# Kernel tuning notes

Measured on AMD Instinct MI355X. Metric: run time of the kernel, lower is better.

The kernel has to match this reference:

```python
import jax, jax.numpy as jnp
import numpy as np

N = 100000
E = 3200000
IN_DIM = 256
OUT_DIM = 256
BN_EPS = 1e-5


def setup_inputs() -> dict:
    key = jax.random.key(0)
    k1, k2, k3, k4, k5 = jax.random.split(key, 5)
    x = jax.random.normal(k1, (N, IN_DIM), dtype=jnp.float32)
    edge_rows = jax.random.randint(k2, (E,), 0, N, dtype=jnp.int32)
    edge_cols = jax.random.randint(k3, (E,), 0, N, dtype=jnp.int32)
    edge_vals = jax.random.uniform(k4, (E,), dtype=jnp.float32)
    # xavier_uniform-like init for weight
    limit = float(np.sqrt(6.0 / (IN_DIM + OUT_DIM)))
    weight = jax.random.uniform(k5, (IN_DIM, OUT_DIM), minval=-limit, maxval=limit, dtype=jnp.float32)
    gamma = jnp.ones((OUT_DIM,), dtype=jnp.float32)
    beta = jnp.zeros((OUT_DIM,), dtype=jnp.float32)
    return {"x": x, "edge_rows": edge_rows, "edge_cols": edge_cols,
            "edge_vals": edge_vals, "weight": weight, "gamma": gamma, "beta": beta}


def reference(x, edge_rows, edge_cols, edge_vals, weight, gamma, beta):
    # dense projection: [N, in] @ [in, out] -> [N, out]
    z = jnp.matmul(x, weight)
    # sparse adjacency matmul (spmm): gather source rows, scale, scatter-add to dest
    msgs = edge_vals[:, None] * z[edge_cols]          # [E, out]
    agg = jax.ops.segment_sum(msgs, edge_rows, num_segments=N)  # [N, out]
    # BatchNorm1d (training mode: batch stats, biased variance) + ReLU
    mean = jnp.mean(agg, axis=0)
    var = jnp.mean(jnp.square(agg - mean), axis=0)
    norm = (agg - mean) * jax.lax.rsqrt(var + BN_EPS) * gamma + beta
    return jax.nn.relu(norm)
```

## Files before the change

### kernel.cpp

```cpp
#include <hip/hip_runtime.h>
#include <hip/hip_bf16.h>

#define N_NODES 100000
#define N_EDGES 3200000
#define DIM 256
#define BN_EPS 1e-5f
#define BROWS 256
#define NBUCK ((N_NODES + BROWS - 1) / BROWS)
#define BIN_BLOCKS 512
#define EPB (N_EDGES / BIN_BLOCKS)
#define RPW 4
#define NPART 64

typedef __attribute__((ext_vector_type(8))) short short8v;
typedef __attribute__((ext_vector_type(4))) float f32x4;

__device__ __forceinline__ float b2f(unsigned short h) {
    return __uint_as_float(((unsigned int)h) << 16);
}
__device__ __forceinline__ unsigned short f2b(float f) {
    unsigned int u = __float_as_uint(f);
    unsigned int rounded = u + 0x7FFF + ((u >> 16) & 1);
    return (unsigned short)(rounded >> 16);
}

__global__ __launch_bounds__(256) void wfrag_kernel(const float* __restrict__ W,
                                                    unsigned short* __restrict__ wfrag) {
    const int t = blockIdx.x * 256 + threadIdx.x;
    const int e = t & 7;
    const int l = (t >> 3) & 63;
    const int frag = t >> 9;
    const int nt = frag >> 3;
    const int ks = frag & 7;
    const int k = ks * 32 + ((l >> 4) << 3) + e;
    const int c = nt * 16 + (l & 15);
    wfrag[t] = f2b(W[k * DIM + c]);
}

__global__ __launch_bounds__(256) void gemm_mfma_kernel(const float* __restrict__ x,
                                                        const unsigned short* __restrict__ wfrag,
                                                        unsigned short* __restrict__ zb) {
    const int wid = (blockIdx.x * blockDim.x + threadIdx.x) >> 6;
    const int lane = threadIdx.x & 63;
    if (wid >= N_NODES / 16) return;
    const int m0 = wid * 16;

    const int arow = m0 + (lane & 15);
    const int kb = (lane >> 4) << 3;
    const float* xrow = x + (size_t)arow * DIM + kb;
    short8v af[8];
    #pragma unroll
    for (int ks = 0; ks < 8; ++ks) {
        const float4 a0 = *(const float4*)(xrow + ks * 32);
        const float4 a1 = *(const float4*)(xrow + ks * 32 + 4);
        short8v f;
        f[0] = (short)f2b(a0.x); f[1] = (short)f2b(a0.y);
        f[2] = (short)f2b(a0.z); f[3] = (short)f2b(a0.w);
        f[4] = (short)f2b(a1.x); f[5] = (short)f2b(a1.y);
        f[6] = (short)f2b(a1.z); f[7] = (short)f2b(a1.w);
        af[ks] = f;
    }

    const int drow0 = m0 + ((lane >> 4) << 2);
    const int dcol = lane & 15;
    for (int nt = 0; nt < 16; ++nt) {
        f32x4 acc = {0.f, 0.f, 0.f, 0.f};
        const unsigned short* wp = wfrag + ((size_t)(nt * 8) * 64 + lane) * 8;
        #pragma unroll
        for (int ks = 0; ks < 8; ++ks) {
            const short8v bf = *(const short8v*)(wp + (size_t)ks * 64 * 8);
            acc = __builtin_amdgcn_mfma_f32_16x16x32_bf16(af[ks], bf, acc, 0, 0, 0);
        }
        unsigned short* zp = zb + (size_t)drow0 * DIM + nt * 16 + dcol;
        zp[0]       = f2b(acc[0]);
        zp[DIM]     = f2b(acc[1]);
        zp[2 * DIM] = f2b(acc[2]);
        zp[3 * DIM] = f2b(acc[3]);
    }
}

__global__ __launch_bounds__(256) void coarse_hist_kernel(const int* __restrict__ rows,
                                                          int* __restrict__ coarse) {
    __shared__ int h[NBUCK];
    const int t = threadIdx.x;
    for (int i = t; i < NBUCK; i += 256) h[i] = 0;
    __syncthreads();
    const int stride = gridDim.x * 256;
    for (int e = blockIdx.x * 256 + t; e < N_EDGES; e += stride)
        atomicAdd(&h[rows[e] >> 8], 1);
    __syncthreads();
    for (int i = t; i < NBUCK; i += 256)
        if (h[i]) atomicAdd(&coarse[i], h[i]);
}

__global__ __launch_bounds__(512) void scan_coarse_kernel(const int* __restrict__ coarse,
                                                          int* __restrict__ coarseBase,
                                                          int* __restrict__ gCursor,
                                                          int* __restrict__ row_ptr) {
    __shared__ int s[512];
    const int t = threadIdx.x;
    const int v = (t < NBUCK) ? coarse[t] : 0;
    s[t] = v;
    __syncthreads();
    for (int off = 1; off < 512; off <<= 1) {
        int x = (t >= off) ? s[t - off] : 0;
        __syncthreads();
        s[t] += x;
        __syncthreads();
    }
    if (t < NBUCK) {
        coarseBase[t] = s[t] - v;
        gCursor[t] = s[t] - v;
    }
    if (t == 0) row_ptr[N_NODES] = N_EDGES;
}

__global__ __launch_bounds__(256) void bin_kernel(const int* __restrict__ rows,
                                                  const int* __restrict__ cols,
                                                  const float* __restrict__ vals,
                                                  int* gCursor,
                                                  int2* __restrict__ gBinned) {
    __shared__ int h[NBUCK];
    __shared__ int base[NBUCK];
    __shared__ int cur[NBUCK];
    const int t = threadIdx.x;
    const int e0 = blockIdx.x * EPB;
    for (int i = t; i < NBUCK; i += 256) h[i] = 0;
    __syncthreads();
    for (int e = e0 + t; e < e0 + EPB; e += 256)
        atomicAdd(&h[rows[e] >> 8], 1);
    __syncthreads();
    for (int b = t; b < NBUCK; b += 256) {
        cur[b] = 0;
        if (h[b]) base[b] = atomicAdd(&gCursor[b], h[b]);
    }
    __syncthreads();
    for (int e = e0 + t; e < e0 + EPB; e += 256) {
        const int r = rows[e];
        const int b = r >> 8;
        const int rk = atomicAdd(&cur[b], 1);
        int2 p;
        p.x = ((r & 255) << 17) | cols[e];
        p.y = __float_as_int(vals[e]);
        gBinned[base[b] + rk] = p;
    }
}

__global__ __launch_bounds__(256) void fine_sort_kernel(const int* __restrict__ coarse,
                                                        const int* __restrict__ coarseBase,
                                                        const int2* __restrict__ gBinned,
                                                        int* __restrict__ row_ptr,
                                                        int2* __restrict__ finalE) {
    __shared__ int h[BROWS];
    __shared__ int s[BROWS];
    __shared__ int cur[BROWS];
    const int t = threadIdx.x;
    const int b = blockIdx.x;
    const int base0 = coarseBase[b];
    const int cnt = coarse[b];
    h[t] = 0;
    __syncthreads();
    for (int e = base0 + t; e < base0 + cnt; e += 256)
        atomicAdd(&h[gBinned[e].x >> 17], 1);
    __syncthreads();
    s[t] = h[t];
    __syncthreads();
    for (int off = 1; off < BROWS; off <<= 1) {
        int x = (t >= off) ? s[t - off] : 0;
        __syncthreads();
        s[t] += x;
        __syncthreads();
    }
    const int excl = s[t] - h[t];
    const int grow = b * BROWS + t;
    if (grow < N_NODES) row_ptr[grow] = base0 + excl;
    cur[t] = excl;
    __syncthreads();
    for (int e = base0 + t; e < base0 + cnt; e += 256) {
        const int2 p = gBinned[e];
        const int rl = p.x >> 17;
        const int rk = atomicAdd(&cur[rl], 1);
        int2 q;
        q.x = p.x & 0x1FFFF;
        q.y = p.y;
        finalE[base0 + rk] = q;
    }
}

__global__ __launch_bounds__(256) void spmm_csr_kernel(const int* __restrict__ row_ptr,
                                                       const int2* __restrict__ pairs,
                                                       const unsigned short* __restrict__ zb,
                                                       float* __restrict__ out,
                                                       float* __restrict__ partials) {
    __shared__ float sdata[2 * DIM];
    const int t = threadIdx.x;
    sdata[t] = 0.f;
    sdata[t + 256] = 0.f;
    __syncthreads();

    const int wave = (blockIdx.x * 256 + t) >> 6;
    const int lane = t & 63;
    const int row0 = wave * RPW;

    float4 s  = make_float4(0.f, 0.f, 0.f, 0.f);
    float4 sq = make_float4(0.f, 0.f, 0.f, 0.f);

    for (int row = row0; row < row0 + RPW; ++row) {
        const int start = __builtin_amdgcn_readfirstlane(row_ptr[row]);
        const int end   = __builtin_amdgcn_readfirstlane(row_ptr[row + 1]);
        float4 acc = make_float4(0.f, 0.f, 0.f, 0.f);
        int2 pA[8], pB[8];
        ushort4 mA[8], mB[8];

#define LOADX(P, M, EB) do { \
    _Pragma("unroll") for (int j = 0; j < 8; ++j) P[j] = pairs[(EB) + j]; \
    _Pragma("unroll") for (int j = 0; j < 8; ++j) \
        M[j] = ((const ushort4*)(zb + (size_t)P[j].x * DIM))[lane]; \
  } while (0)
#define FMAX(P, M) do { \
    _Pragma("unroll") for (int j = 0; j < 8; ++j) { \
        const float v = __int_as_float(P[j].y); \
        acc.x += v * b2f(M[j].x); \
        acc.y += v * b2f(M[j].y); \
        acc.z += v * b2f(M[j].z); \
        acc.w += v * b2f(M[j].w); \
    } \
  } while (0)

        const int nb = (end - start) >> 3;
        int e = start;
        if (nb) {
            LOADX(pA, mA, e); e += 8;
            int b = 1;
            for (; b + 1 < nb; b += 2) {
                LOADX(pB, mB, e); e += 8;
                FMAX(pA, mA);
                LOADX(pA, mA, e); e += 8;
                FMAX(pB, mB);
            }
            if (b < nb) {
                LOADX(pB, mB, e); e += 8;
                FMAX(pA, mA);
                FMAX(pB, mB);
            } else {
                FMAX(pA, mA);
            }
        }
        const int rem = end - e;
        if (rem) {
            #pragma unroll
            for (int j = 0; j < 8; ++j) if (j < rem) pA[j] = pairs[e + j];
            #pragma unroll
            for (int j = 0; j < 8; ++j) if (j < rem)
                mA[j] = ((const ushort4*)(zb + (size_t)pA[j].x * DIM))[lane];
            #pragma unroll
            for (int j = 0; j < 8; ++j) if (j < rem) {
                const float v = __int_as_float(pA[j].y);
                acc.x += v * b2f(mA[j].x);
                acc.y += v * b2f(mA[j].y);
                acc.z += v * b2f(mA[j].z);
                acc.w += v * b2f(mA[j].w);
            }
        }
#undef LOADX
#undef FMAX

        f32x4 st = {acc.x, acc.y, acc.z, acc.w};
        __builtin_nontemporal_store(st, (f32x4*)(out + (size_t)row * DIM) + lane);

        s.x += acc.x; s.y += acc.y; s.z += acc.z; s.w += acc.w;
        sq.x += acc.x * acc.x; sq.y += acc.y * acc.y;
        sq.z += acc.z * acc.z; sq.w += acc.w * acc.w;
    }

    const int c0 = lane * 4;
    atomicAdd(&sdata[c0 + 0], s.x);
    atomicAdd(&sdata[c0 + 1], s.y);
    atomicAdd(&sdata[c0 + 2], s.z);
    atomicAdd(&sdata[c0 + 3], s.w);
    atomicAdd(&sdata[256 + c0 + 0], sq.x);
    atomicAdd(&sdata[256 + c0 + 1], sq.y);
    atomicAdd(&sdata[256 + c0 + 2], sq.z);
    atomicAdd(&sdata[256 + c0 + 3], sq.w);
    __syncthreads();

    float* pb = partials + (size_t)(blockIdx.x & (NPART - 1)) * (2 * DIM);
    atomicAdd(&pb[t], sdata[t]);
    atomicAdd(&pb[t + 256], sdata[t + 256]);
}

__global__ __launch_bounds__(256) void finalize_kernel(const float* __restrict__ partials,
                                                       const float* __restrict__ gamma,
                                                       const float* __restrict__ beta,
                                                       float* __restrict__ sb) {
    const int c = threadIdx.x;
    float s = 0.f, ssq = 0.f;
    for (int b = 0; b < NPART; ++b) {
        s   += partials[b * (2 * DIM) + c];
        ssq += partials[b * (2 * DIM) + 256 + c];
    }
    const float inv_n = 1.0f / (float)N_NODES;
    const float mean = s * inv_n;
    float var = ssq * inv_n - mean * mean;
    const float rstd = rsqrtf(var + BN_EPS);
    const float scale = rstd * gamma[c];
    sb[c] = scale;
    sb[DIM + c] = beta[c] - mean * scale;
}

#define NORM_BLOCKS 2048
__global__ __launch_bounds__(256) void norm_kernel(float* __restrict__ out,
                                                   const float* __restrict__ sb) {
    const int c0 = (threadIdx.x & 63) * 4;
    const float s0 = sb[c0 + 0], s1 = sb[c0 + 1], s2 = sb[c0 + 2], s3 = sb[c0 + 3];
    const float b0 = sb[DIM + c0 + 0], b1 = sb[DIM + c0 + 1];
    const float b2 = sb[DIM + c0 + 2], b3 = sb[DIM + c0 + 3];
    const int nvec = N_NODES * (DIM / 4);
    for (int idx = blockIdx.x * 256 + threadIdx.x; idx < nvec; idx += NORM_BLOCKS * 256) {
        float4 a = ((float4*)out)[idx];
        float4 o;
        o.x = fmaxf(fmaf(a.x, s0, b0), 0.f);
        o.y = fmaxf(fmaf(a.y, s1, b1), 0.f);
        o.z = fmaxf(fmaf(a.z, s2, b2), 0.f);
        o.w = fmaxf(fmaf(a.w, s3, b3), 0.f);
        ((float4*)out)[idx] = o;
    }
}

extern "C" void kernel_launch(void* const* d_in, const int* in_sizes, int n_in,
                              void* d_out, int out_size, void* d_ws, size_t ws_size,
                              hipStream_t stream) {
    const float* x         = (const float*)d_in[0];
    const int*   edge_rows = (const int*)d_in[1];
    const int*   edge_cols = (const int*)d_in[2];
    const float* edge_vals = (const float*)d_in[3];
    const float* weight    = (const float*)d_in[4];
    const float* gamma     = (const float*)d_in[5];
    const float* beta      = (const float*)d_in[6];
    float* out = (float*)d_out;

    unsigned short* zb    = (unsigned short*)d_ws;
    unsigned short* wfrag = zb + (size_t)N_NODES * DIM;
    int2*  gBinned  = (int2*)(wfrag + DIM * DIM);
    int2*  finalE   = gBinned + N_EDGES;
    int*   row_ptr  = (int*)(finalE + N_EDGES);
    int*   coarse   = row_ptr + N_NODES + 1;
    float* partials = (float*)(coarse + 392);
    float* sb       = partials + NPART * 2 * DIM;
    int*   coarseBase = (int*)(sb + 2 * DIM);
    int*   gCursor  = coarseBase + 392;

    hipMemsetAsync(coarse, 0, (392 + NPART * 2 * DIM) * sizeof(int), stream);

    wfrag_kernel<<<DIM * DIM / 256, 256, 0, stream>>>(weight, wfrag);
    gemm_mfma_kernel<<<(N_NODES / 16 + 3) / 4, 256, 0, stream>>>(x, wfrag, zb);

    coarse_hist_kernel<<<BIN_BLOCKS, 256, 0, stream>>>(edge_rows, coarse);
    scan_coarse_kernel<<<1, 512, 0, stream>>>(coarse, coarseBase, gCursor, row_ptr);
    bin_kernel<<<BIN_BLOCKS, 256, 0, stream>>>(edge_rows, edge_cols, edge_vals, gCursor, gBinned);
    fine_sort_kernel<<<NBUCK, 256, 0, stream>>>(coarse, coarseBase, gBinned, row_ptr, finalE);

    spmm_csr_kernel<<<N_NODES / (RPW * 4), 256, 0, stream>>>(row_ptr, finalE, zb, out, partials);

    finalize_kernel<<<1, 256, 0, stream>>>(partials, gamma, beta, sb);
    norm_kernel<<<NORM_BLOCKS, 256, 0, stream>>>(out, sb);
}
```

Baseline: 485.0 us.

## Split SpMM into two column-half passes to shrink gather working set

The CSR SpMM now runs as two launches, each handling 128 of the 256 output columns. Every lane gathers a ushort2 instead of a ushort4. The gathered slice of the bf16 feature table per pass is half as large, which is meant to improve L2/MALL hit rates on the random row gathers. In exchange the edge list and row pointers are read twice, there is an extra launch, and each gather moves fewer bytes, so per-edge overhead goes up.

```diff
diff --git a/kernel.cpp b/kernel.cpp
--- a/kernel.cpp
+++ b/kernel.cpp
@@ -14,6 +14,7 @@
 
 typedef __attribute__((ext_vector_type(8))) short short8v;
 typedef __attribute__((ext_vector_type(4))) float f32x4;
+typedef __attribute__((ext_vector_type(2))) float f32x2;
 
 __device__ __forceinline__ float b2f(unsigned short h) {
     return __uint_as_float(((unsigned int)h) << 16);
@@ -191,7 +192,8 @@
                                                        const int2* __restrict__ pairs,
                                                        const unsigned short* __restrict__ zb,
                                                        float* __restrict__ out,
-                                                       float* __restrict__ partials) {
+                                                       float* __restrict__ partials,
+                                                       const int hh) {
     __shared__ float sdata[2 * DIM];
     const int t = threadIdx.x;
     sdata[t] = 0.f;
@@ -201,29 +203,28 @@
     const int wave = (blockIdx.x * 256 + t) >> 6;
     const int lane = t & 63;
     const int row0 = wave * RPW;
-
-    float4 s  = make_float4(0.f, 0.f, 0.f, 0.f);
-    float4 sq = make_float4(0.f, 0.f, 0.f, 0.f);
+    const int cb = hh << 7;
+
+    f32x2 s  = {0.f, 0.f};
+    f32x2 sq = {0.f, 0.f};
 
     for (int row = row0; row < row0 + RPW; ++row) {
         const int start = __builtin_amdgcn_readfirstlane(row_ptr[row]);
         const int end   = __builtin_amdgcn_readfirstlane(row_ptr[row + 1]);
-        float4 acc = make_float4(0.f, 0.f, 0.f, 0.f);
+        f32x2 acc = {0.f, 0.f};
         int2 pA[8], pB[8];
-        ushort4 mA[8], mB[8];
+        ushort2 mA[8], mB[8];
 
 #define LOADX(P, M, EB) do { \
     _Pragma("unroll") for (int j = 0; j < 8; ++j) P[j] = pairs[(EB) + j]; \
     _Pragma("unroll") for (int j = 0; j < 8; ++j) \
-        M[j] = ((const ushort4*)(zb + (size_t)P[j].x * DIM))[lane]; \
+        M[j] = ((const ushort2*)(zb + (size_t)P[j].x * DIM + cb))[lane]; \
   } while (0)
 #define FMAX(P, M) do { \
     _Pragma("unroll") for (int j = 0; j < 8; ++j) { \
         const float v = __int_as_float(P[j].y); \
         acc.x += v * b2f(M[j].x); \
         acc.y += v * b2f(M[j].y); \
-        acc.z += v * b2f(M[j].z); \
-        acc.w += v * b2f(M[j].w); \
     } \
   } while (0)
 
@@ -252,41 +253,37 @@
             for (int j = 0; j < 8; ++j) if (j < rem) pA[j] = pairs[e + j];
             #pragma unroll
             for (int j = 0; j < 8; ++j) if (j < rem)
-                mA[j] = ((const ushort4*)(zb + (size_t)pA[j].x * DIM))[lane];
+                mA[j] = ((const ushort2*)(zb + (size_t)pA[j].x * DIM + cb))[lane];
             #pragma unroll
             for (int j = 0; j < 8; ++j) if (j < rem) {
                 const float v = __int_as_float(pA[j].y);
                 acc.x += v * b2f(mA[j].x);
                 acc.y += v * b2f(mA[j].y);
-                acc.z += v * b2f(mA[j].z);
-                acc.w += v * b2f(mA[j].w);
             }
         }
 #undef LOADX
 #undef FMAX
 
-        f32x4 st = {acc.x, acc.y, acc.z, acc.w};
-        __builtin_nontemporal_store(st, (f32x4*)(out + (size_t)row * DIM) + lane);
-
-        s.x += acc.x; s.y += acc.y; s.z += acc.z; s.w += acc.w;
+        __builtin_nontemporal_store(acc, (f32x2*)(out + (size_t)row * DIM + cb) + lane);
+
+        s.x += acc.x; s.y += acc.y;
         sq.x += acc.x * acc.x; sq.y += acc.y * acc.y;
-        sq.z += acc.z * acc.z; sq.w += acc.w * acc.w;
-    }
-
-    const int c0 = lane * 4;
+    }
+
+    const int c0 = cb + lane * 2;
     atomicAdd(&sdata[c0 + 0], s.x);
     atomicAdd(&sdata[c0 + 1], s.y);
-    atomicAdd(&sdata[c0 + 2], s.z);
-    atomicAdd(&sdata[c0 + 3], s.w);
     atomicAdd(&sdata[256 + c0 + 0], sq.x);
     atomicAdd(&sdata[256 + c0 + 1], sq.y);
-    atomicAdd(&sdata[256 + c0 + 2], sq.z);
-    atomicAdd(&sdata[256 + c0 + 3], sq.w);
     __syncthreads();
 
     float* pb = partials + (size_t)(blockIdx.x & (NPART - 1)) * (2 * DIM);
-    atomicAdd(&pb[t], sdata[t]);
-    atomicAdd(&pb[t + 256], sdata[t + 256]);
+    if (t < 128) {
+        atomicAdd(&pb[cb + t], sdata[cb + t]);
+    } else if (t < 256) {
+        const int i = 256 + cb + (t - 128);
+        atomicAdd(&pb[i], sdata[i]);
+    }
 }
 
 __global__ __launch_bounds__(256) void finalize_kernel(const float* __restrict__ partials,
@@ -360,7 +357,8 @@
     bin_kernel<<<BIN_BLOCKS, 256, 0, stream>>>(edge_rows, edge_cols, edge_vals, gCursor, gBinned);
     fine_sort_kernel<<<NBUCK, 256, 0, stream>>>(coarse, coarseBase, gBinned, row_ptr, finalE);
 
-    spmm_csr_kernel<<<N_NODES / (RPW * 4), 256, 0, stream>>>(row_ptr, finalE, zb, out, partials);
+    spmm_csr_kernel<<<N_NODES / (RPW * 4), 256, 0, stream>>>(row_ptr, finalE, zb, out, partials, 0);
+    spmm_csr_kernel<<<N_NODES / (RPW * 4), 256, 0, stream>>>(row_ptr, finalE, zb, out, partials, 1);
 
     finalize_kernel<<<1, 256, 0, stream>>>(partials, gamma, beta, sb);
     norm_kernel<<<NORM_BLOCKS, 256, 0, stream>>>(out, sb);
```

Result: slower. 504.4 us (+4.0%).

## Replace histogram+scan with fixed-capacity bucket slots and per-row end pointers

Applied to the files above, without the earlier changes.

Removes the coarse histogram pass and the single-block scan kernel. The bin kernel now writes each bucket of 256 rows into a fixed slot of CAP entries, using an atomic per-bucket counter as the cursor. The fine sort emits separate row_ptr and row_end arrays, and the SpMM reads its row end from row_end. The binned scratch reuses the zb workspace region, so binning runs before the GEMM. This saves one full read of edge_rows and two launches, but silently overflows if any bucket gets more than CAP edges, which could happen with skewed degree distributions.

```diff
diff --git a/kernel.cpp b/kernel.cpp
--- a/kernel.cpp
+++ b/kernel.cpp
@@ -11,6 +11,7 @@
 #define EPB (N_EDGES / BIN_BLOCKS)
 #define RPW 4
 #define NPART 64
+#define CAP 10240
 
 typedef __attribute__((ext_vector_type(8))) short short8v;
 typedef __attribute__((ext_vector_type(4))) float f32x4;
@@ -79,46 +80,10 @@
     }
 }
 
-__global__ __launch_bounds__(256) void coarse_hist_kernel(const int* __restrict__ rows,
-                                                          int* __restrict__ coarse) {
-    __shared__ int h[NBUCK];
-    const int t = threadIdx.x;
-    for (int i = t; i < NBUCK; i += 256) h[i] = 0;
-    __syncthreads();
-    const int stride = gridDim.x * 256;
-    for (int e = blockIdx.x * 256 + t; e < N_EDGES; e += stride)
-        atomicAdd(&h[rows[e] >> 8], 1);
-    __syncthreads();
-    for (int i = t; i < NBUCK; i += 256)
-        if (h[i]) atomicAdd(&coarse[i], h[i]);
-}
-
-__global__ __launch_bounds__(512) void scan_coarse_kernel(const int* __restrict__ coarse,
-                                                          int* __restrict__ coarseBase,
-                                                          int* __restrict__ gCursor,
-                                                          int* __restrict__ row_ptr) {
-    __shared__ int s[512];
-    const int t = threadIdx.x;
-    const int v = (t < NBUCK) ? coarse[t] : 0;
-    s[t] = v;
-    __syncthreads();
-    for (int off = 1; off < 512; off <<= 1) {
-        int x = (t >= off) ? s[t - off] : 0;
-        __syncthreads();
-        s[t] += x;
-        __syncthreads();
-    }
-    if (t < NBUCK) {
-        coarseBase[t] = s[t] - v;
-        gCursor[t] = s[t] - v;
-    }
-    if (t == 0) row_ptr[N_NODES] = N_EDGES;
-}
-
 __global__ __launch_bounds__(256) void bin_kernel(const int* __restrict__ rows,
                                                   const int* __restrict__ cols,
                                                   const float* __restrict__ vals,
-                                                  int* gCursor,
+                                                  int* bucketCnt,
                                                   int2* __restrict__ gBinned) {
     __shared__ int h[NBUCK];
     __shared__ int base[NBUCK];
@@ -132,7 +97,7 @@
     __syncthreads();
     for (int b = t; b < NBUCK; b += 256) {
         cur[b] = 0;
-        if (h[b]) base[b] = atomicAdd(&gCursor[b], h[b]);
+        if (h[b]) base[b] = atomicAdd(&bucketCnt[b], h[b]);
     }
     __syncthreads();
     for (int e = e0 + t; e < e0 + EPB; e += 256) {
@@ -142,22 +107,22 @@
         int2 p;
         p.x = ((r & 255) << 17) | cols[e];
         p.y = __float_as_int(vals[e]);
-        gBinned[base[b] + rk] = p;
-    }
-}
-
-__global__ __launch_bounds__(256) void fine_sort_kernel(const int* __restrict__ coarse,
-                                                        const int* __restrict__ coarseBase,
+        gBinned[(size_t)b * CAP + base[b] + rk] = p;
+    }
+}
+
+__global__ __launch_bounds__(256) void fine_sort_kernel(const int* __restrict__ bucketCnt,
                                                         const int2* __restrict__ gBinned,
                                                         int* __restrict__ row_ptr,
+                                                        int* __restrict__ row_end,
                                                         int2* __restrict__ finalE) {
     __shared__ int h[BROWS];
     __shared__ int s[BROWS];
     __shared__ int cur[BROWS];
     const int t = threadIdx.x;
     const int b = blockIdx.x;
-    const int base0 = coarseBase[b];
-    const int cnt = coarse[b];
+    const int base0 = b * CAP;
+    const int cnt = bucketCnt[b];
     h[t] = 0;
     __syncthreads();
     for (int e = base0 + t; e < base0 + cnt; e += 256)
@@ -173,7 +138,10 @@
     }
     const int excl = s[t] - h[t];
     const int grow = b * BROWS + t;
-    if (grow < N_NODES) row_ptr[grow] = base0 + excl;
+    if (grow < N_NODES) {
+        row_ptr[grow] = base0 + excl;
+        row_end[grow] = base0 + s[t];
+    }
     cur[t] = excl;
     __syncthreads();
     for (int e = base0 + t; e < base0 + cnt; e += 256) {
@@ -188,6 +156,7 @@
 }
 
 __global__ __launch_bounds__(256) void spmm_csr_kernel(const int* __restrict__ row_ptr,
+                                                       const int* __restrict__ row_end,
                                                        const int2* __restrict__ pairs,
                                                        const unsigned short* __restrict__ zb,
                                                        float* __restrict__ out,
@@ -207,7 +176,7 @@
 
     for (int row = row0; row < row0 + RPW; ++row) {
         const int start = __builtin_amdgcn_readfirstlane(row_ptr[row]);
-        const int end   = __builtin_amdgcn_readfirstlane(row_ptr[row + 1]);
+        const int end   = __builtin_amdgcn_readfirstlane(row_end[row]);
         float4 acc = make_float4(0.f, 0.f, 0.f, 0.f);
         int2 pA[8], pB[8];
         ushort4 mA[8], mB[8];
@@ -340,27 +309,24 @@
     float* out = (float*)d_out;
 
     unsigned short* zb    = (unsigned short*)d_ws;
+    int2*  gBinned  = (int2*)d_ws;
     unsigned short* wfrag = zb + (size_t)N_NODES * DIM;
-    int2*  gBinned  = (int2*)(wfrag + DIM * DIM);
-    int2*  finalE   = gBinned + N_EDGES;
-    int*   row_ptr  = (int*)(finalE + N_EDGES);
-    int*   coarse   = row_ptr + N_NODES + 1;
-    float* partials = (float*)(coarse + 392);
+    int2*  finalE   = (int2*)(wfrag + DIM * DIM);
+    int*   row_ptr  = (int*)(finalE + (size_t)NBUCK * CAP);
+    int*   row_end  = row_ptr + N_NODES;
+    int*   bucketCnt = row_end + N_NODES;
+    float* partials = (float*)(bucketCnt + NBUCK);
     float* sb       = partials + NPART * 2 * DIM;
-    int*   coarseBase = (int*)(sb + 2 * DIM);
-    int*   gCursor  = coarseBase + 392;
-
-    hipMemsetAsync(coarse, 0, (392 + NPART * 2 * DIM) * sizeof(int), stream);
+
+    hipMemsetAsync(bucketCnt, 0, (NBUCK + NPART * 2 * DIM) * sizeof(int), stream);
+
+    bin_kernel<<<BIN_BLOCKS, 256, 0, stream>>>(edge_rows, edge_cols, edge_vals, bucketCnt, gBinned);
+    fine_sort_kernel<<<NBUCK, 256, 0, stream>>>(bucketCnt, gBinned, row_ptr, row_end, finalE);
 
     wfrag_kernel<<<DIM * DIM / 256, 256, 0, stream>>>(weight, wfrag);
     gemm_mfma_kernel<<<(N_NODES / 16 + 3) / 4, 256, 0, stream>>>(x, wfrag, zb);
 
-    coarse_hist_kernel<<<BIN_BLOCKS, 256, 0, stream>>>(edge_rows, coarse);
-    scan_coarse_kernel<<<1, 512, 0, stream>>>(coarse, coarseBase, gCursor, row_ptr);
-    bin_kernel<<<BIN_BLOCKS, 256, 0, stream>>>(edge_rows, edge_cols, edge_vals, gCursor, gBinned);
-    fine_sort_kernel<<<NBUCK, 256, 0, stream>>>(coarse, coarseBase, gBinned, row_ptr, finalE);
-
-    spmm_csr_kernel<<<N_NODES / (RPW * 4), 256, 0, stream>>>(row_ptr, finalE, zb, out, partials);
+    spmm_csr_kernel<<<N_NODES / (RPW * 4), 256, 0, stream>>>(row_ptr, row_end, finalE, zb, out, partials);
 
     finalize_kernel<<<1, 256, 0, stream>>>(partials, gamma, beta, sb);
     norm_kernel<<<NORM_BLOCKS, 256, 0, stream>>>(out, sb);
```

Result: faster. 454.2 us (-6.3%).
